# Optimization experiments

Measured on AMD Instinct MI355X. Metric: run time of the kernel, lower is better.

Reference implementation:

```python
import jax, jax.numpy as jnp
import numpy as np

B, S, E = 4, 2880, 512
BLOCK = 64
TOP_K = 8


def setup_inputs() -> dict:
    key = jax.random.key(0)
    k1, k2, k3 = jax.random.split(key, 3)
    x = jax.random.normal(k1, (B, S, E), dtype=jnp.float32)
    phi = jax.random.normal(k2, (1, 1, E), dtype=jnp.float32)          # num_heads=1 -> head_dim=E
    pos_emb = jax.random.normal(k3, (S, E), dtype=jnp.float32)         # nn.Embedding(SEQ_LEN, E) table
    return {"x": x, "phi": phi, "pos_emb": pos_emb}


def _block_sparse_mask(phi, seq_len):
    """Replicates apply_sparse_attention: block-diagonal coarse mask ANDed with
    rows selected by per-column top-k of the phi outer-product similarity.
    All blocks are full (seq_len % BLOCK == 0) so the per-block pattern is shared.
    Returns (mask[S,S] bool, row_sel[S] bool)."""
    p = phi[0, 0, :BLOCK]                       # phi[:, :, :block_size]
    sim = p[:, None] * p[None, :]               # [BLOCK, BLOCK] outer-product similarity
    _, idx = jax.lax.top_k(sim.T, TOP_K)        # top-k along dim 0 per column -> [BLOCK, TOP_K]
    sel = jnp.zeros((BLOCK,), bool).at[idx.reshape(-1)].set(True)  # union of selected rows
    r = jnp.arange(seq_len)
    same_block = (r[:, None] // BLOCK) == (r[None, :] // BLOCK)    # coarse block-diagonal mask
    row_sel = sel[r % BLOCK]                    # fine mask: whole rows enabled
    return same_block & row_sel[:, None], row_sel


def reference(x, phi, pos_emb):
    b, s, e = x.shape
    head_dim = e                                 # num_heads = 1
    q = x + pos_emb[None] + phi                  # [B,S,E]
    scores = jnp.einsum('bse,bte->bst', q, q) / jnp.sqrt(jnp.float32(head_dim))
    mask, row_sel = _block_sparse_mask(phi, s)
    neg = jnp.finfo(scores.dtype).min
    scores = jnp.where(mask[None], scores, neg)
    probs = jax.nn.softmax(scores, axis=-1)
    probs = jnp.where(row_sel[None, :, None], probs, 0.0)  # fully-masked rows -> zero weights
    out = jnp.einsum('bst,bte->bse', probs, x)   # attention-weighted values
    return out
```

## Files before the change

kernel.cpp:

```cpp
#include <hip/hip_runtime.h>

#define NBLOCKS 45
#define NBATCH  4
#define SEQ     2880
#define EMB     512
#define BLK     64

typedef __attribute__((ext_vector_type(8))) short short8;
typedef __attribute__((ext_vector_type(4))) float floatx4;

#define QSTR 264
#define XSTR 88
#define PSTR 72
#define SSTR 65

__device__ __forceinline__ unsigned short f2bf(float f) {
    unsigned int x = __float_as_uint(f);
    unsigned int r = (x + 0x7fffu + ((x >> 16) & 1u)) >> 16;
    return (unsigned short)r;
}

__device__ __forceinline__ unsigned long long topk8_mask(float v, int lane) {
    unsigned long long res = 0ull;
    bool alive = true;
    for (int k = 0; k < 8; ++k) {
        float bv = alive ? v : -__builtin_inff();
        int bi = lane;
        #pragma unroll
        for (int off = 1; off < 64; off <<= 1) {
            float ov = __shfl_xor(bv, off);
            int oi = __shfl_xor(bi, off);
            if (ov > bv || (ov == bv && oi < bi)) { bv = ov; bi = oi; }
        }
        res |= 1ull << bi;
        if (lane == bi) alive = false;
    }
    return res;
}

__global__ __launch_bounds__(512) void nsparse_attn(
    const float* __restrict__ x,
    const float* __restrict__ phi,
    const float* __restrict__ pos,
    float* __restrict__ out)
{
    __shared__ __align__(16) unsigned char s_buf[256 * XSTR * 2];
    __shared__ __align__(16) unsigned short s_P[BLK * PSTR];
    __shared__ int s_sel[BLK];

    const int tid  = threadIdx.x;
    const int wave = tid >> 6;
    const int lane = tid & 63;
    const int quad = lane >> 4;
    const int lcol = lane & 15;

    const int nb = blockIdx.x;
    const int b  = blockIdx.y;
    const int t0 = nb * BLK;

    const float* xb = x + ((size_t)b * SEQ + t0) * EMB;
    float* ob = out + ((size_t)b * SEQ + t0) * EMB;

    if (wave == 0) {
        float pv = phi[lane];
        unsigned long long bp = __ballot(pv > 0.0f);
        unsigned long long bn = __ballot(pv < 0.0f);
        unsigned long long bz = __ballot(pv == 0.0f);
        unsigned long long selm = 0ull;
        if (bz) selm |= 0xffull;
        if (bp) selm |= topk8_mask(pv, lane);
        if (bn) selm |= topk8_mask(-pv, lane);
        s_sel[lane] = (int)((selm >> lane) & 1ull);
    }

    unsigned short* qb = (unsigned short*)s_buf;
    const int mi  = wave >> 1;
    const int ni0 = (wave & 1) * 2;

    floatx4 accS0 = {0.f, 0.f, 0.f, 0.f};
    floatx4 accS1 = {0.f, 0.f, 0.f, 0.f};

    for (int kc = 0; kc < 2; ++kc) {
        if (kc) __syncthreads();
        const int e0 = kc * 256;
        #pragma unroll
        for (int k = 0; k < 8; ++k) {
            const int r = wave + 8 * k;
            const float4 xv = *(const float4*)(xb  + (size_t)r * EMB + e0 + lane * 4);
            const float4 pv = *(const float4*)(pos + (size_t)(t0 + r) * EMB + e0 + lane * 4);
            const float4 fv = *(const float4*)(phi + e0 + lane * 4);
            unsigned short u0 = f2bf(xv.x + pv.x + fv.x);
            unsigned short u1 = f2bf(xv.y + pv.y + fv.y);
            unsigned short u2 = f2bf(xv.z + pv.z + fv.z);
            unsigned short u3 = f2bf(xv.w + pv.w + fv.w);
            unsigned int w0 = (unsigned int)u0 | ((unsigned int)u1 << 16);
            unsigned int w1 = (unsigned int)u2 | ((unsigned int)u3 << 16);
            *(uint2*)&qb[r * QSTR + lane * 4] = make_uint2(w0, w1);
        }
        __syncthreads();
        #pragma unroll
        for (int ks = 0; ks < 8; ++ks) {
            const int koff = ks * 32 + quad * 8;
            short8 a  = *(const short8*)&qb[(mi  * 16 + lcol) * QSTR + koff];
            short8 b0 = *(const short8*)&qb[(ni0 * 16 + lcol) * QSTR + koff];
            short8 b1 = *(const short8*)&qb[((ni0 + 1) * 16 + lcol) * QSTR + koff];
            accS0 = __builtin_amdgcn_mfma_f32_16x16x32_bf16(a, b0, accS0, 0, 0, 0);
            accS1 = __builtin_amdgcn_mfma_f32_16x16x32_bf16(a, b1, accS1, 0, 0, 0);
        }
    }
    __syncthreads();

    float* Sb = (float*)s_buf;
    const float scale = 0.044194173824159216f;
    #pragma unroll
    for (int r = 0; r < 4; ++r) {
        const int row = mi * 16 + quad * 4 + r;
        Sb[row * SSTR + (ni0       * 16 + lcol)] = accS0[r] * scale;
        Sb[row * SSTR + ((ni0 + 1) * 16 + lcol)] = accS1[r] * scale;
    }
    __syncthreads();

    {
        const int srow = tid >> 3;
        const int sj = tid & 7;
        float v[8];
        float m = -__builtin_inff();
        #pragma unroll
        for (int i = 0; i < 8; ++i) {
            v[i] = Sb[srow * SSTR + sj + 8 * i];
            m = fmaxf(m, v[i]);
        }
        #pragma unroll
        for (int off = 1; off < 8; off <<= 1) m = fmaxf(m, __shfl_xor(m, off));
        float s = 0.f;
        #pragma unroll
        for (int i = 0; i < 8; ++i) { v[i] = __expf(v[i] - m); s += v[i]; }
        #pragma unroll
        for (int off = 1; off < 8; off <<= 1) s += __shfl_xor(s, off);
        const float inv = 1.0f / s;
        #pragma unroll
        for (int i = 0; i < 8; ++i) s_P[srow * PSTR + sj + 8 * i] = f2bf(v[i] * inv);
    }
    __syncthreads();

    unsigned short* xT = (unsigned short*)s_buf;
    for (int ec = 0; ec < 2; ++ec) {
        if (ec) __syncthreads();
        const int e0 = ec * 256;
        #pragma unroll
        for (int k = 0; k < 8; ++k) {
            const int c4 = wave + 8 * k;
            const float4 xv = *(const float4*)(xb + (size_t)lane * EMB + e0 + c4 * 4);
            xT[(c4 * 4 + 0) * XSTR + lane] = f2bf(xv.x);
            xT[(c4 * 4 + 1) * XSTR + lane] = f2bf(xv.y);
            xT[(c4 * 4 + 2) * XSTR + lane] = f2bf(xv.z);
            xT[(c4 * 4 + 3) * XSTR + lane] = f2bf(xv.w);
        }
        __syncthreads();
        short8 a0 = *(const short8*)&s_P[(mi * 16 + lcol) * PSTR + 0 + quad * 8];
        short8 a1 = *(const short8*)&s_P[(mi * 16 + lcol) * PSTR + 32 + quad * 8];
        #pragma unroll
        for (int j = 0; j < 8; ++j) {
            const int nt = (wave & 1) + 2 * j;
            short8 bf0 = *(const short8*)&xT[(nt * 16 + lcol) * XSTR + 0 + quad * 8];
            short8 bf1 = *(const short8*)&xT[(nt * 16 + lcol) * XSTR + 32 + quad * 8];
            floatx4 acc = {0.f, 0.f, 0.f, 0.f};
            acc = __builtin_amdgcn_mfma_f32_16x16x32_bf16(a0, bf0, acc, 0, 0, 0);
            acc = __builtin_amdgcn_mfma_f32_16x16x32_bf16(a1, bf1, acc, 0, 0, 0);
            #pragma unroll
            for (int r = 0; r < 4; ++r) {
                const int row = mi * 16 + quad * 4 + r;
                const int col = e0 + nt * 16 + lcol;
                ob[(size_t)row * EMB + col] = s_sel[row] ? acc[r] : 0.0f;
            }
        }
    }
}

extern "C" void kernel_launch(void* const* d_in, const int* in_sizes, int n_in,
                              void* d_out, int out_size, void* d_ws, size_t ws_size,
                              hipStream_t stream) {
    const float* x   = (const float*)d_in[0];
    const float* phi = (const float*)d_in[1];
    const float* pos = (const float*)d_in[2];
    float* out = (float*)d_out;
    dim3 grid(NBLOCKS, NBATCH);
    hipLaunchKernelGGL(nsparse_attn, grid, dim3(512), 0, stream, x, phi, pos, out);
}
```

Baseline: 103.4 us.

## Compute attention only for selected rows and zero-fill unselected output rows

Builds a compacted list of the selected rows in each block and runs the QK^T score MFMAs, softmax and PV MFMAs only over those rows, padded to 16-row tiles. Unselected output rows are written as zeros with vectorized float4 stores. The first half of the x transpose is overlapped with softmax by splitting waves between the two tasks, bf16 packing now uses the library conversion, and the LDS strides change. This trades fixed full-block compute for data-dependent loops, more barriers and scattered row stores.

```diff
diff --git a/kernel.cpp b/kernel.cpp
--- a/kernel.cpp
+++ b/kernel.cpp
@@ -1,4 +1,5 @@
 #include <hip/hip_runtime.h>
+#include <hip/hip_bf16.h>
 
 #define NBLOCKS 45
 #define NBATCH  4
@@ -10,14 +11,20 @@
 typedef __attribute__((ext_vector_type(4))) float floatx4;
 
 #define QSTR 264
-#define XSTR 88
+#define XSTR 72
 #define PSTR 72
-#define SSTR 65
+#define SSTR 66
 
 __device__ __forceinline__ unsigned short f2bf(float f) {
     unsigned int x = __float_as_uint(f);
     unsigned int r = (x + 0x7fffu + ((x >> 16) & 1u)) >> 16;
     return (unsigned short)r;
+}
+
+__device__ __forceinline__ unsigned int pk2bf(float a, float b) {
+    __hip_bfloat162 h = __float22bfloat162_rn(make_float2(a, b));
+    union { __hip_bfloat162 h; unsigned int u; } cv; cv.h = h;
+    return cv.u;
 }
 
 __device__ __forceinline__ unsigned long long topk8_mask(float v, int lane) {
@@ -45,8 +52,11 @@
     float* __restrict__ out)
 {
     __shared__ __align__(16) unsigned char s_buf[256 * XSTR * 2];
-    __shared__ __align__(16) unsigned short s_P[BLK * PSTR];
+    __shared__ __align__(16) float s_S[32 * SSTR];
+    __shared__ __align__(16) unsigned short s_Pc[32 * PSTR];
     __shared__ int s_sel[BLK];
+    __shared__ int s_glist[32];
+    __shared__ int s_m;
 
     const int tid  = threadIdx.x;
     const int wave = tid >> 6;
@@ -71,107 +81,190 @@
         if (bp) selm |= topk8_mask(pv, lane);
         if (bn) selm |= topk8_mask(-pv, lane);
         s_sel[lane] = (int)((selm >> lane) & 1ull);
+        if (lane < 32) s_glist[lane] = 0;
+        if (lane == 0) s_m = __popcll(selm);
+        if ((selm >> lane) & 1ull) {
+            int rank = __popcll(selm & ((1ull << lane) - 1ull));
+            s_glist[rank] = lane;
+        }
     }
 
     unsigned short* qb = (unsigned short*)s_buf;
-    const int mi  = wave >> 1;
-    const int ni0 = (wave & 1) * 2;
-
-    floatx4 accS0 = {0.f, 0.f, 0.f, 0.f};
-    floatx4 accS1 = {0.f, 0.f, 0.f, 0.f};
-
-    for (int kc = 0; kc < 2; ++kc) {
-        if (kc) __syncthreads();
-        const int e0 = kc * 256;
+
+    {
         #pragma unroll
         for (int k = 0; k < 8; ++k) {
             const int r = wave + 8 * k;
-            const float4 xv = *(const float4*)(xb  + (size_t)r * EMB + e0 + lane * 4);
-            const float4 pv = *(const float4*)(pos + (size_t)(t0 + r) * EMB + e0 + lane * 4);
-            const float4 fv = *(const float4*)(phi + e0 + lane * 4);
-            unsigned short u0 = f2bf(xv.x + pv.x + fv.x);
-            unsigned short u1 = f2bf(xv.y + pv.y + fv.y);
-            unsigned short u2 = f2bf(xv.z + pv.z + fv.z);
-            unsigned short u3 = f2bf(xv.w + pv.w + fv.w);
-            unsigned int w0 = (unsigned int)u0 | ((unsigned int)u1 << 16);
-            unsigned int w1 = (unsigned int)u2 | ((unsigned int)u3 << 16);
-            *(uint2*)&qb[r * QSTR + lane * 4] = make_uint2(w0, w1);
-        }
-        __syncthreads();
+            const float4 xv = *(const float4*)(xb  + (size_t)r * EMB + lane * 4);
+            const float4 pv = *(const float4*)(pos + (size_t)(t0 + r) * EMB + lane * 4);
+            const float4 fv = *(const float4*)(phi + lane * 4);
+            uint2 w2;
+            w2.x = pk2bf(xv.x + pv.x + fv.x, xv.y + pv.y + fv.y);
+            w2.y = pk2bf(xv.z + pv.z + fv.z, xv.w + pv.w + fv.w);
+            *(uint2*)&qb[r * QSTR + lane * 4] = w2;
+        }
+    }
+    __syncthreads();
+
+    const int m  = s_m;
+    const int NT = (m + 15) >> 4;
+    const int mi = wave >> 2;
+    const int ni = wave & 3;
+    const bool a_on = (mi < NT);
+    int a_row = 0;
+    if (a_on) a_row = s_glist[mi * 16 + lcol];
+
+    floatx4 accS = {0.f, 0.f, 0.f, 0.f};
+    if (a_on) {
         #pragma unroll
         for (int ks = 0; ks < 8; ++ks) {
             const int koff = ks * 32 + quad * 8;
-            short8 a  = *(const short8*)&qb[(mi  * 16 + lcol) * QSTR + koff];
-            short8 b0 = *(const short8*)&qb[(ni0 * 16 + lcol) * QSTR + koff];
-            short8 b1 = *(const short8*)&qb[((ni0 + 1) * 16 + lcol) * QSTR + koff];
-            accS0 = __builtin_amdgcn_mfma_f32_16x16x32_bf16(a, b0, accS0, 0, 0, 0);
-            accS1 = __builtin_amdgcn_mfma_f32_16x16x32_bf16(a, b1, accS1, 0, 0, 0);
-        }
-    }
-    __syncthreads();
-
-    float* Sb = (float*)s_buf;
-    const float scale = 0.044194173824159216f;
-    #pragma unroll
-    for (int r = 0; r < 4; ++r) {
-        const int row = mi * 16 + quad * 4 + r;
-        Sb[row * SSTR + (ni0       * 16 + lcol)] = accS0[r] * scale;
-        Sb[row * SSTR + ((ni0 + 1) * 16 + lcol)] = accS1[r] * scale;
-    }
-    __syncthreads();
-
-    {
-        const int srow = tid >> 3;
+            short8 a  = *(const short8*)&qb[a_row * QSTR + koff];
+            short8 bb = *(const short8*)&qb[(ni * 16 + lcol) * QSTR + koff];
+            accS = __builtin_amdgcn_mfma_f32_16x16x32_bf16(a, bb, accS, 0, 0, 0);
+        }
+    }
+
+    {
+        const float4 z4 = {0.f, 0.f, 0.f, 0.f};
+        #pragma unroll
+        for (int it = 0; it < 16; ++it) {
+            const int idx = tid + it * 512;
+            const int r = idx >> 7, c4 = idx & 127;
+            if (!s_sel[r]) *(float4*)(ob + (size_t)r * EMB + c4 * 4) = z4;
+        }
+    }
+    __syncthreads();
+
+    {
+        #pragma unroll
+        for (int k = 0; k < 8; ++k) {
+            const int r = wave + 8 * k;
+            const float4 xv = *(const float4*)(xb  + (size_t)r * EMB + 256 + lane * 4);
+            const float4 pv = *(const float4*)(pos + (size_t)(t0 + r) * EMB + 256 + lane * 4);
+            const float4 fv = *(const float4*)(phi + 256 + lane * 4);
+            uint2 w2;
+            w2.x = pk2bf(xv.x + pv.x + fv.x, xv.y + pv.y + fv.y);
+            w2.y = pk2bf(xv.z + pv.z + fv.z, xv.w + pv.w + fv.w);
+            *(uint2*)&qb[r * QSTR + lane * 4] = w2;
+        }
+    }
+    __syncthreads();
+
+    if (a_on) {
+        #pragma unroll
+        for (int ks = 0; ks < 8; ++ks) {
+            const int koff = ks * 32 + quad * 8;
+            short8 a  = *(const short8*)&qb[a_row * QSTR + koff];
+            short8 bb = *(const short8*)&qb[(ni * 16 + lcol) * QSTR + koff];
+            accS = __builtin_amdgcn_mfma_f32_16x16x32_bf16(a, bb, accS, 0, 0, 0);
+        }
+        const float scale = 0.044194173824159216f;
+        #pragma unroll
+        for (int r = 0; r < 4; ++r) {
+            const int g = mi * 16 + quad * 4 + r;
+            s_S[g * SSTR + ni * 16 + lcol] = accS[r] * scale;
+        }
+    }
+    __syncthreads();
+
+    unsigned short* xT = (unsigned short*)s_buf;
+
+    if (tid < NT * 128) {
+        const int g = tid >> 3;
         const int sj = tid & 7;
         float v[8];
-        float m = -__builtin_inff();
+        float mx = -__builtin_inff();
         #pragma unroll
         for (int i = 0; i < 8; ++i) {
-            v[i] = Sb[srow * SSTR + sj + 8 * i];
-            m = fmaxf(m, v[i]);
-        }
-        #pragma unroll
-        for (int off = 1; off < 8; off <<= 1) m = fmaxf(m, __shfl_xor(m, off));
+            v[i] = s_S[g * SSTR + sj + 8 * i];
+            mx = fmaxf(mx, v[i]);
+        }
+        #pragma unroll
+        for (int off = 1; off < 8; off <<= 1) mx = fmaxf(mx, __shfl_xor(mx, off));
         float s = 0.f;
         #pragma unroll
-        for (int i = 0; i < 8; ++i) { v[i] = __expf(v[i] - m); s += v[i]; }
+        for (int i = 0; i < 8; ++i) { v[i] = __expf(v[i] - mx); s += v[i]; }
         #pragma unroll
         for (int off = 1; off < 8; off <<= 1) s += __shfl_xor(s, off);
         const float inv = 1.0f / s;
         #pragma unroll
-        for (int i = 0; i < 8; ++i) s_P[srow * PSTR + sj + 8 * i] = f2bf(v[i] * inv);
-    }
-    __syncthreads();
-
-    unsigned short* xT = (unsigned short*)s_buf;
-    for (int ec = 0; ec < 2; ++ec) {
-        if (ec) __syncthreads();
-        const int e0 = ec * 256;
-        #pragma unroll
-        for (int k = 0; k < 8; ++k) {
-            const int c4 = wave + 8 * k;
-            const float4 xv = *(const float4*)(xb + (size_t)lane * EMB + e0 + c4 * 4);
+        for (int i = 0; i < 8; ++i) s_Pc[g * PSTR + sj + 8 * i] = f2bf(v[i] * inv);
+    } else if (wave >= 4) {
+        #pragma unroll
+        for (int k = 0; k < 16; ++k) {
+            const int c4 = (wave - 4) + 4 * k;
+            const float4 xv = *(const float4*)(xb + (size_t)lane * EMB + c4 * 4);
             xT[(c4 * 4 + 0) * XSTR + lane] = f2bf(xv.x);
             xT[(c4 * 4 + 1) * XSTR + lane] = f2bf(xv.y);
             xT[(c4 * 4 + 2) * XSTR + lane] = f2bf(xv.z);
             xT[(c4 * 4 + 3) * XSTR + lane] = f2bf(xv.w);
         }
-        __syncthreads();
-        short8 a0 = *(const short8*)&s_P[(mi * 16 + lcol) * PSTR + 0 + quad * 8];
-        short8 a1 = *(const short8*)&s_P[(mi * 16 + lcol) * PSTR + 32 + quad * 8];
-        #pragma unroll
-        for (int j = 0; j < 8; ++j) {
-            const int nt = (wave & 1) + 2 * j;
-            short8 bf0 = *(const short8*)&xT[(nt * 16 + lcol) * XSTR + 0 + quad * 8];
-            short8 bf1 = *(const short8*)&xT[(nt * 16 + lcol) * XSTR + 32 + quad * 8];
+    }
+    __syncthreads();
+
+    #pragma unroll 1
+    for (int mi3 = 0; mi3 < NT; ++mi3) {
+        const short8 a0 = *(const short8*)&s_Pc[(mi3 * 16 + lcol) * PSTR + 0  + quad * 8];
+        const short8 a1 = *(const short8*)&s_Pc[(mi3 * 16 + lcol) * PSTR + 32 + quad * 8];
+        int rows[4]; bool val[4];
+        #pragma unroll
+        for (int r = 0; r < 4; ++r) {
+            const int g = mi3 * 16 + quad * 4 + r;
+            rows[r] = s_glist[g];
+            val[r] = (g < m);
+        }
+        #pragma unroll
+        for (int jj = 0; jj < 2; ++jj) {
+            const int nt = wave + 8 * jj;
+            const short8 b0 = *(const short8*)&xT[(nt * 16 + lcol) * XSTR + 0  + quad * 8];
+            const short8 b1 = *(const short8*)&xT[(nt * 16 + lcol) * XSTR + 32 + quad * 8];
             floatx4 acc = {0.f, 0.f, 0.f, 0.f};
-            acc = __builtin_amdgcn_mfma_f32_16x16x32_bf16(a0, bf0, acc, 0, 0, 0);
-            acc = __builtin_amdgcn_mfma_f32_16x16x32_bf16(a1, bf1, acc, 0, 0, 0);
+            acc = __builtin_amdgcn_mfma_f32_16x16x32_bf16(a0, b0, acc, 0, 0, 0);
+            acc = __builtin_amdgcn_mfma_f32_16x16x32_bf16(a1, b1, acc, 0, 0, 0);
             #pragma unroll
             for (int r = 0; r < 4; ++r) {
-                const int row = mi * 16 + quad * 4 + r;
-                const int col = e0 + nt * 16 + lcol;
-                ob[(size_t)row * EMB + col] = s_sel[row] ? acc[r] : 0.0f;
+                if (val[r]) ob[(size_t)rows[r] * EMB + nt * 16 + lcol] = acc[r];
+            }
+        }
+    }
+    __syncthreads();
+
+    {
+        #pragma unroll
+        for (int k = 0; k < 8; ++k) {
+            const int c4 = wave + 8 * k;
+            const float4 xv = *(const float4*)(xb + (size_t)lane * EMB + 256 + c4 * 4);
+            xT[(c4 * 4 + 0) * XSTR + lane] = f2bf(xv.x);
+            xT[(c4 * 4 + 1) * XSTR + lane] = f2bf(xv.y);
+            xT[(c4 * 4 + 2) * XSTR + lane] = f2bf(xv.z);
+            xT[(c4 * 4 + 3) * XSTR + lane] = f2bf(xv.w);
+        }
+    }
+    __syncthreads();
+
+    #pragma unroll 1
+    for (int mi3 = 0; mi3 < NT; ++mi3) {
+        const short8 a0 = *(const short8*)&s_Pc[(mi3 * 16 + lcol) * PSTR + 0  + quad * 8];
+        const short8 a1 = *(const short8*)&s_Pc[(mi3 * 16 + lcol) * PSTR + 32 + quad * 8];
+        int rows[4]; bool val[4];
+        #pragma unroll
+        for (int r = 0; r < 4; ++r) {
+            const int g = mi3 * 16 + quad * 4 + r;
+            rows[r] = s_glist[g];
+            val[r] = (g < m);
+        }
+        #pragma unroll
+        for (int jj = 0; jj < 2; ++jj) {
+            const int nt = wave + 8 * jj;
+            const short8 b0 = *(const short8*)&xT[(nt * 16 + lcol) * XSTR + 0  + quad * 8];
+            const short8 b1 = *(const short8*)&xT[(nt * 16 + lcol) * XSTR + 32 + quad * 8];
+            floatx4 acc = {0.f, 0.f, 0.f, 0.f};
+            acc = __builtin_amdgcn_mfma_f32_16x16x32_bf16(a0, b0, acc, 0, 0, 0);
+            acc = __builtin_amdgcn_mfma_f32_16x16x32_bf16(a1, b1, acc, 0, 0, 0);
+            #pragma unroll
+            for (int r = 0; r < 4; ++r) {
+                if (val[r]) ob[(size_t)rows[r] * EMB + 256 + nt * 16 + lcol] = acc[r];
             }
         }
     }
```

Measured after the change: 96.05 us. 1.08x faster.
